# Kernel tuning notes

Hardware: AMD Instinct MI355X
Metric: run time of the kernel (lower is better)

## Reference

```python
import jax, jax.numpy as jnp
import numpy as np


def _lstm_layer(x, lengths, w_ih, w_hh, b):
    # x: [B, T, D], lengths: [B] int, w_ih/w_hh: [4H, D/H], b: [4H]
    B, T, D = x.shape
    H = w_hh.shape[1]
    # precompute input projection for all timesteps: [T, B, 4H]
    gx = (jnp.einsum('btd,gd->btg', x, w_ih) + b).transpose(1, 0, 2)
    tmask = (jnp.arange(T)[:, None] < lengths[None, :])[:, :, None]  # [T, B, 1]

    def step(carry, inp):
        c, h = carry
        g_x, m = inp
        gates = g_x + h @ w_hh.T  # [B, 4H]
        f, i, o, cg = jnp.split(gates, 4, axis=1)
        f = jax.nn.sigmoid(f)
        i = jax.nn.sigmoid(i)
        o = jax.nn.sigmoid(o)
        cg = jnp.tanh(cg)
        c_next = f * c + i * cg
        h_next = o * jnp.tanh(c_next)
        c_next = jnp.where(m, c_next, c)
        h_next = jnp.where(m, h_next, h)
        return (c_next, h_next), h_next

    c0 = jnp.zeros((B, H), dtype=x.dtype)
    h0 = jnp.zeros((B, H), dtype=x.dtype)
    (c_f, h_f), hs = jax.lax.scan(step, (c0, h0), (gx, tmask))
    return hs.transpose(1, 0, 2), (c_f, h_f)  # [B, T, H]


def reference(x, lengths, w_ih_0, w_hh_0, b_0, w_ih_1, w_hh_1, b_1):
    out0, (c0, h0) = _lstm_layer(x, lengths, w_ih_0, w_hh_0, b_0)
    out1, (c1, h1) = _lstm_layer(out0, lengths, w_ih_1, w_hh_1, b_1)
    c = jnp.stack([c0, c1], 0)  # [num_layers, B, H]
    h = jnp.stack([h0, h1], 0)
    return out1, (c, h)


def setup_inputs() -> dict:
    key = jax.random.key(0)
    ks = jax.random.split(key, 6)
    B, T, D, H = 32, 512, 1024, 1024
    s_in = 1.0 / np.sqrt(D)
    s_h = 1.0 / np.sqrt(H)
    return {
        'x': jax.random.normal(ks[0], (B, T, D), jnp.float32),
        'lengths': jax.random.randint(ks[1], (B,), 0, T).astype(jnp.int64),
        'w_ih_0': jax.random.normal(ks[2], (4 * H, D), jnp.float32) * s_in,
        'w_hh_0': jax.random.normal(ks[3], (4 * H, H), jnp.float32) * s_h,
        'b_0': jnp.zeros((4 * H,), jnp.float32),
        'w_ih_1': jax.random.normal(ks[4], (4 * H, H), jnp.float32) * s_h,
        'w_hh_1': jax.random.normal(ks[5], (4 * H, H), jnp.float32) * s_h,
        'b_1': jnp.zeros((4 * H,), jnp.float32),
    }
```

## Files before the change

### kernel.cpp

```cpp
#include <hip/hip_runtime.h>


#define BB 32
#define TT 512
#define HH 1024
#define NBLK 128

typedef float f32x4 __attribute__((ext_vector_type(4)));
typedef __bf16 bf16x8 __attribute__((ext_vector_type(8)));
typedef unsigned int u32x4 __attribute__((ext_vector_type(4)));

#define H0_OFF  0
#define H1_OFF  33554432
#define FL0_OFF 67108864
#define FL1_OFF (67108864 + 512)

#define LD16(d, a) asm volatile("global_load_dwordx4 %0, %1, off sc0 sc1" \
                                : "=v"(d) : "v"(a) : "memory")
#define ST16(a, v) asm volatile("global_store_dwordx4 %0, %1, off sc0 sc1" \
                                :: "v"(a), "v"(v) : "memory")

__device__ __forceinline__ float sigm(float x){ return 1.f/(1.f+__expf(-x)); }
__device__ __forceinline__ float tanh_s(float x){
  float a = fminf(fabsf(x), 20.f);
  float e = __expf(2.f*a);
  float r = (e-1.f)/(e+1.f);
  return x < 0.f ? -r : r;
}

__device__ __forceinline__ void waitflag(const int* fl, int lane, int need){
  const int* p = fl + 2*lane;
  for (;;){
    int a = __hip_atomic_load(p,   __ATOMIC_RELAXED, __HIP_MEMORY_SCOPE_AGENT);
    int b = __hip_atomic_load(p+1, __ATOMIC_RELAXED, __HIP_MEMORY_SCOPE_AGENT);
    if (!__any((a < need) | (b < need))) return;
    __builtin_amdgcn_s_sleep(1);
  }
}

__global__ __launch_bounds__(256, 1) void lstm2(
    const float* __restrict__ x, const int* __restrict__ l32,
    const float* __restrict__ wih0, const float* __restrict__ whh0, const float* __restrict__ b0,
    const float* __restrict__ wih1, const float* __restrict__ whh1, const float* __restrict__ b1,
    float* __restrict__ out, char* __restrict__ ws)
{
  extern __shared__ char smem[];
  float* redf = (float*)(smem + 131072);
  __bf16* hstage = (__bf16*)(smem + 149504);
  const int tid = threadIdx.x, bid = blockIdx.x;
  const int layer = bid >> 7, lb = bid & (NBLK-1), c0 = lb*8;
  const float* wih  = layer ? wih1 : wih0;
  const float* whh  = layer ? whh1 : whh0;
  const float* bias = layer ? b1 : b0;
  __bf16* h0b = (__bf16*)(ws + H0_OFF);
  __bf16* h1b = (__bf16*)(ws + H1_OFF);
  int* fl0 = (int*)(ws + FL0_OFF);
  int* fl1 = (int*)(ws + FL1_OFF);

  for (int idx = tid; idx < 32*1024; idx += 256){
    int m = idx >> 10, k = idx & (HH-1);
    int gr = (m >> 3)*HH + c0 + (m & 7);
    int off = m*2048 + ((k*2) ^ ((m & 15) << 4));
    *(__bf16*)(smem + off)         = (__bf16)wih[(size_t)gr*HH + k];
    *(__bf16*)(smem + 65536 + off) = (__bf16)whh[(size_t)gr*HH + k];
  }

  int odd = 0;
#pragma unroll
  for (int i = 1; i < 32; i += 2) odd |= l32[i];
  const int eb = tid >> 3, ec = tid & 7, cgl = c0 + ec;
  const int mylen = odd ? l32[eb] : l32[2*eb];
  float bias_r[4];
#pragma unroll
  for (int g = 0; g < 4; ++g) bias_r[g] = bias[g*HH + cgl];
  float c_st = 0.f, h_st = 0.f;

  const int lane = tid & 63, wid = tid >> 6;
  const int part = wid >> 1;
  const int kch  = wid & 1;
  const int col16 = lane & 15, kgrp = lane >> 4;
  const int axor = col16 << 4;
  const char* wbase = (const char*)smem + part*65536 + col16*2048 + kch*1024;
  float* wr = redf + wid*1152;
  const int kbase = kch*512 + kgrp*8;

  __syncthreads();

  for (int t = 0; t < TT; ++t){
    f32x4 acc00={0,0,0,0}, acc01={0,0,0,0}, acc10={0,0,0,0}, acc11={0,0,0,0};

    const __bf16* bsrc = nullptr;
    const float*  fsrc = nullptr;
    const int* fl = nullptr; int need = 0;
    if (layer == 0){
      if (part == 0) fsrc = x + (t << 10);
      else if (t > 0){ bsrc = h0b + ((size_t)(t-1) << 15); fl = fl0; need = t; }
    } else {
      if (part == 0){ bsrc = h0b + ((size_t)t << 15); fl = fl0; need = t+1; }
      else if (t > 0){ bsrc = h1b + ((size_t)(t-1) << 15); fl = fl1; need = t; }
    }
    if (fl) waitflag(fl, lane, need);

    if (bsrc){
      const char* pa = (const char*)(bsrc + col16*HH + kbase);
      const char* pb = (const char*)(bsrc + (16+col16)*HH + kbase);
      u32x4 ra[16], rb[16];
#pragma unroll
      for (int u = 0; u < 16; ++u){ LD16(ra[u], pa + u*64); LD16(rb[u], pb + u*64); }
      asm volatile("s_waitcnt vmcnt(0)" ::: "memory");
      __builtin_amdgcn_sched_barrier(0);
#pragma unroll
      for (int u = 0; u < 16; ++u){
        bf16x8 bv0 = __builtin_bit_cast(bf16x8, ra[u]);
        bf16x8 bv1 = __builtin_bit_cast(bf16x8, rb[u]);
        int ao = (u*64 + kgrp*16) ^ axor;
        bf16x8 a0 = *(const bf16x8*)(wbase + ao);
        bf16x8 a1 = *(const bf16x8*)(wbase + 32768 + ao);
        acc00 = __builtin_amdgcn_mfma_f32_16x16x32_bf16(a0, bv0, acc00, 0,0,0);
        acc01 = __builtin_amdgcn_mfma_f32_16x16x32_bf16(a0, bv1, acc01, 0,0,0);
        acc10 = __builtin_amdgcn_mfma_f32_16x16x32_bf16(a1, bv0, acc10, 0,0,0);
        acc11 = __builtin_amdgcn_mfma_f32_16x16x32_bf16(a1, bv1, acc11, 0,0,0);
      }
    } else if (fsrc){
      const float* p0 = fsrc + ((size_t)col16 << 19) + kbase;
      const float* p1 = fsrc + ((size_t)(16+col16) << 19) + kbase;
#pragma unroll 4
      for (int kb = 0; kb < 16; ++kb){
        float4 u0a = *(const float4*)(p0 + kb*32), u0b = *(const float4*)(p0 + kb*32 + 4);
        float4 u1a = *(const float4*)(p1 + kb*32), u1b = *(const float4*)(p1 + kb*32 + 4);
        bf16x8 bv0, bv1;
        bv0[0]=(__bf16)u0a.x; bv0[1]=(__bf16)u0a.y; bv0[2]=(__bf16)u0a.z; bv0[3]=(__bf16)u0a.w;
        bv0[4]=(__bf16)u0b.x; bv0[5]=(__bf16)u0b.y; bv0[6]=(__bf16)u0b.z; bv0[7]=(__bf16)u0b.w;
        bv1[0]=(__bf16)u1a.x; bv1[1]=(__bf16)u1a.y; bv1[2]=(__bf16)u1a.z; bv1[3]=(__bf16)u1a.w;
        bv1[4]=(__bf16)u1b.x; bv1[5]=(__bf16)u1b.y; bv1[6]=(__bf16)u1b.z; bv1[7]=(__bf16)u1b.w;
        int ao = (kb*64 + kgrp*16) ^ axor;
        bf16x8 a0 = *(const bf16x8*)(wbase + ao);
        bf16x8 a1 = *(const bf16x8*)(wbase + 32768 + ao);
        acc00 = __builtin_amdgcn_mfma_f32_16x16x32_bf16(a0, bv0, acc00, 0,0,0);
        acc01 = __builtin_amdgcn_mfma_f32_16x16x32_bf16(a0, bv1, acc01, 0,0,0);
        acc10 = __builtin_amdgcn_mfma_f32_16x16x32_bf16(a1, bv0, acc10, 0,0,0);
        acc11 = __builtin_amdgcn_mfma_f32_16x16x32_bf16(a1, bv1, acc11, 0,0,0);
      }
    }

    *(f32x4*)(wr + col16*36 + kgrp*4)           = acc00;
    *(f32x4*)(wr + (16+col16)*36 + kgrp*4)      = acc01;
    *(f32x4*)(wr + col16*36 + 16 + kgrp*4)      = acc10;
    *(f32x4*)(wr + (16+col16)*36 + 16 + kgrp*4) = acc11;
    __syncthreads();

    float vv[4];
#pragma unroll
    for (int g = 0; g < 4; ++g){
      int mi = eb*36 + g*8 + ec;
      vv[g] = redf[mi] + redf[1152+mi] + redf[2304+mi] + redf[3456+mi] + bias_r[g];
    }
    float fg = sigm(vv[0]), ig = sigm(vv[1]), og = sigm(vv[2]), gg = tanh_s(vv[3]);
    float cn = fg*c_st + ig*gg;
    float hn = og*tanh_s(cn);
    if (t < mylen){ c_st = cn; h_st = hn; }
    hstage[eb*8 + ec] = (__bf16)h_st;
    if (layer) out[((size_t)(eb*TT + t) << 10) + cgl] = h_st;
    __syncthreads();

    if (wid == 0){
      __bf16* hb = (layer ? h1b : h0b) + ((size_t)t << 15) + c0;
      if (lane < 32){
        u32x4 hv = *(const u32x4*)(hstage + lane*8);
        ST16(hb + (size_t)lane*HH, hv);
      }
      asm volatile("s_waitcnt vmcnt(0)" ::: "memory");
      if (lane == 0)
        __hip_atomic_store((layer ? fl1 : fl0) + lb, t+1,
                           __ATOMIC_RELAXED, __HIP_MEMORY_SCOPE_AGENT);
    }
  }

  const size_t OFFC = (size_t)BB*TT*HH;
  out[OFFC + (layer << 15) + (eb << 10) + cgl] = c_st;
  out[OFFC + ((2 + layer) << 15) + (eb << 10) + cgl] = h_st;
}

extern "C" void kernel_launch(void* const* d_in, const int* in_sizes, int n_in,
                              void* d_out, int out_size, void* d_ws, size_t ws_size,
                              hipStream_t stream) {
  const float* x    = (const float*)d_in[0];
  const int*   lens = (const int*)d_in[1];
  const float* wih0 = (const float*)d_in[2];
  const float* whh0 = (const float*)d_in[3];
  const float* b0   = (const float*)d_in[4];
  const float* wih1 = (const float*)d_in[5];
  const float* whh1 = (const float*)d_in[6];
  const float* b1   = (const float*)d_in[7];
  float* out = (float*)d_out;
  char* ws = (char*)d_ws;

  (void)hipMemsetAsync(ws + FL0_OFF, 0, 1024, stream);

  const int lds_bytes = 131072 + 4*1152*4 + 512;
  (void)hipFuncSetAttribute((const void*)lstm2,
                            hipFuncAttributeMaxDynamicSharedMemorySize, lds_bytes);
  lstm2<<<dim3(256), dim3(256), lds_bytes, stream>>>(
      x, lens, wih0, whh0, b0, wih1, whh1, b1, out, ws);
}
```

Before: 5.805 ms.

## Use per-timestep arrival counters, pre-converted bf16 input, and a ring buffer for layer-1 h

Replaces the per-block flag array, which every wave scanned across 128 entries, with one atomic counter per timestep. Each block increments the counter after publishing its slice of h, and waiters poll a single word until it reaches 128. A separate pre-pass converts x to bf16 in a [T,B,D] layout, so layer 0 reads x through the same bf16 MFMA path as h instead of doing strided fp32 loads and conversions inside the recurrent loop. Layer-1 hidden states go into a 4-slot ring with a padded row stride, and the data loads drop the sc0/sc1 coherence bits. That last change risks stale reads across caches, particularly for the reused ring slots.

```diff
diff --git a/kernel.cpp b/kernel.cpp
--- a/kernel.cpp
+++ b/kernel.cpp
@@ -5,18 +5,20 @@
 #define TT 512
 #define HH 1024
 #define NBLK 128
+#define TSTR 66048
 
 typedef float f32x4 __attribute__((ext_vector_type(4)));
 typedef __bf16 bf16x8 __attribute__((ext_vector_type(8)));
+typedef __bf16 bf16x4 __attribute__((ext_vector_type(4)));
 typedef unsigned int u32x4 __attribute__((ext_vector_type(4)));
 
-#define H0_OFF  0
-#define H1_OFF  33554432
-#define FL0_OFF 67108864
-#define FL1_OFF (67108864 + 512)
+#define H0_OFF   0
+#define H1R_OFF  33816576
+#define CNT_OFF  34080768
+#define XBF_OFF  34084864
 
-#define LD16(d, a) asm volatile("global_load_dwordx4 %0, %1, off sc0 sc1" \
-                                : "=v"(d) : "v"(a) : "memory")
+#define LDC16(d, a) asm volatile("global_load_dwordx4 %0, %1, off" \
+                                 : "=v"(d) : "v"(a) : "memory")
 #define ST16(a, v) asm volatile("global_store_dwordx4 %0, %1, off sc0 sc1" \
                                 :: "v"(a), "v"(v) : "memory")
 
@@ -27,19 +29,29 @@
   float r = (e-1.f)/(e+1.f);
   return x < 0.f ? -r : r;
 }
+__device__ __forceinline__ int ld_coh(const int* p){
+  int v;
+  asm volatile("global_load_dword %0, %1, off sc0 sc1\n\ts_waitcnt vmcnt(0)"
+               : "=v"(v) : "v"(p) : "memory");
+  return v;
+}
+__device__ __forceinline__ void poll128(const int* p){
+  while (ld_coh(p) < NBLK) __builtin_amdgcn_s_sleep(1);
+}
 
-__device__ __forceinline__ void waitflag(const int* fl, int lane, int need){
-  const int* p = fl + 2*lane;
-  for (;;){
-    int a = __hip_atomic_load(p,   __ATOMIC_RELAXED, __HIP_MEMORY_SCOPE_AGENT);
-    int b = __hip_atomic_load(p+1, __ATOMIC_RELAXED, __HIP_MEMORY_SCOPE_AGENT);
-    if (!__any((a < need) | (b < need))) return;
-    __builtin_amdgcn_s_sleep(1);
-  }
+__global__ __launch_bounds__(256) void xconv_kernel(const float* __restrict__ x,
+                                                    __bf16* __restrict__ xbf){
+  int i = blockIdx.x*256 + threadIdx.x;
+  int flat = i << 2;
+  int b = flat >> 19, t = (flat >> 10) & (TT-1), d = flat & (HH-1);
+  float4 v = *(const float4*)(x + flat);
+  bf16x4 o;
+  o[0]=(__bf16)v.x; o[1]=(__bf16)v.y; o[2]=(__bf16)v.z; o[3]=(__bf16)v.w;
+  *(bf16x4*)(xbf + ((t*BB + b) << 10) + d) = o;
 }
 
 __global__ __launch_bounds__(256, 1) void lstm2(
-    const float* __restrict__ x, const int* __restrict__ l32,
+    const int* __restrict__ l32,
     const float* __restrict__ wih0, const float* __restrict__ whh0, const float* __restrict__ b0,
     const float* __restrict__ wih1, const float* __restrict__ whh1, const float* __restrict__ b1,
     float* __restrict__ out, char* __restrict__ ws)
@@ -52,10 +64,11 @@
   const float* wih  = layer ? wih1 : wih0;
   const float* whh  = layer ? whh1 : whh0;
   const float* bias = layer ? b1 : b0;
-  __bf16* h0b = (__bf16*)(ws + H0_OFF);
-  __bf16* h1b = (__bf16*)(ws + H1_OFF);
-  int* fl0 = (int*)(ws + FL0_OFF);
-  int* fl1 = (int*)(ws + FL1_OFF);
+  char* h0 = ws + H0_OFF;
+  char* h1r = ws + H1R_OFF;
+  int* cnt0 = (int*)(ws + CNT_OFF);
+  int* cnt1 = cnt0 + 512;
+  const char* xb = ws + XBF_OFF;
 
   for (int idx = tid; idx < 32*1024; idx += 256){
     int m = idx >> 10, k = idx & (HH-1);
@@ -89,24 +102,23 @@
   for (int t = 0; t < TT; ++t){
     f32x4 acc00={0,0,0,0}, acc01={0,0,0,0}, acc10={0,0,0,0}, acc11={0,0,0,0};
 
-    const __bf16* bsrc = nullptr;
-    const float*  fsrc = nullptr;
-    const int* fl = nullptr; int need = 0;
+    const char* sb = nullptr;
+    const int* pollp = nullptr;
     if (layer == 0){
-      if (part == 0) fsrc = x + (t << 10);
-      else if (t > 0){ bsrc = h0b + ((size_t)(t-1) << 15); fl = fl0; need = t; }
+      if (part == 0) sb = xb + ((size_t)t << 16);
+      else if (t > 0){ sb = h0 + (size_t)(t-1)*TSTR; pollp = cnt0 + (t-1); }
     } else {
-      if (part == 0){ bsrc = h0b + ((size_t)t << 15); fl = fl0; need = t+1; }
-      else if (t > 0){ bsrc = h1b + ((size_t)(t-1) << 15); fl = fl1; need = t; }
+      if (part == 0){ sb = h0 + (size_t)t*TSTR; pollp = cnt0 + t; }
+      else if (t > 0){ sb = h1r + (size_t)((t-1)&3)*TSTR; pollp = cnt1 + (t-1); }
     }
-    if (fl) waitflag(fl, lane, need);
+    if (pollp) poll128(pollp);
 
-    if (bsrc){
-      const char* pa = (const char*)(bsrc + col16*HH + kbase);
-      const char* pb = (const char*)(bsrc + (16+col16)*HH + kbase);
+    if (sb){
+      const char* pa = sb + col16*2048 + kbase*2;
+      const char* pb = sb + (16+col16)*2048 + kbase*2;
       u32x4 ra[16], rb[16];
 #pragma unroll
-      for (int u = 0; u < 16; ++u){ LD16(ra[u], pa + u*64); LD16(rb[u], pb + u*64); }
+      for (int u = 0; u < 16; ++u){ LDC16(ra[u], pa + u*64); LDC16(rb[u], pb + u*64); }
       asm volatile("s_waitcnt vmcnt(0)" ::: "memory");
       __builtin_amdgcn_sched_barrier(0);
 #pragma unroll
@@ -114,26 +126,6 @@
         bf16x8 bv0 = __builtin_bit_cast(bf16x8, ra[u]);
         bf16x8 bv1 = __builtin_bit_cast(bf16x8, rb[u]);
         int ao = (u*64 + kgrp*16) ^ axor;
-        bf16x8 a0 = *(const bf16x8*)(wbase + ao);
-        bf16x8 a1 = *(const bf16x8*)(wbase + 32768 + ao);
-        acc00 = __builtin_amdgcn_mfma_f32_16x16x32_bf16(a0, bv0, acc00, 0,0,0);
-        acc01 = __builtin_amdgcn_mfma_f32_16x16x32_bf16(a0, bv1, acc01, 0,0,0);
-        acc10 = __builtin_amdgcn_mfma_f32_16x16x32_bf16(a1, bv0, acc10, 0,0,0);
-        acc11 = __builtin_amdgcn_mfma_f32_16x16x32_bf16(a1, bv1, acc11, 0,0,0);
-      }
-    } else if (fsrc){
-      const float* p0 = fsrc + ((size_t)col16 << 19) + kbase;
-      const float* p1 = fsrc + ((size_t)(16+col16) << 19) + kbase;
-#pragma unroll 4
-      for (int kb = 0; kb < 16; ++kb){
-        float4 u0a = *(const float4*)(p0 + kb*32), u0b = *(const float4*)(p0 + kb*32 + 4);
-        float4 u1a = *(const float4*)(p1 + kb*32), u1b = *(const float4*)(p1 + kb*32 + 4);
-        bf16x8 bv0, bv1;
-        bv0[0]=(__bf16)u0a.x; bv0[1]=(__bf16)u0a.y; bv0[2]=(__bf16)u0a.z; bv0[3]=(__bf16)u0a.w;
-        bv0[4]=(__bf16)u0b.x; bv0[5]=(__bf16)u0b.y; bv0[6]=(__bf16)u0b.z; bv0[7]=(__bf16)u0b.w;
-        bv1[0]=(__bf16)u1a.x; bv1[1]=(__bf16)u1a.y; bv1[2]=(__bf16)u1a.z; bv1[3]=(__bf16)u1a.w;
-        bv1[4]=(__bf16)u1b.x; bv1[5]=(__bf16)u1b.y; bv1[6]=(__bf16)u1b.z; bv1[7]=(__bf16)u1b.w;
-        int ao = (kb*64 + kgrp*16) ^ axor;
         bf16x8 a0 = *(const bf16x8*)(wbase + ao);
         bf16x8 a1 = *(const bf16x8*)(wbase + 32768 + ao);
         acc00 = __builtin_amdgcn_mfma_f32_16x16x32_bf16(a0, bv0, acc00, 0,0,0);
@@ -164,15 +156,15 @@
     __syncthreads();
 
     if (wid == 0){
-      __bf16* hb = (layer ? h1b : h0b) + ((size_t)t << 15) + c0;
+      char* hb = (layer ? (h1r + (size_t)(t&3)*TSTR) : (h0 + (size_t)t*TSTR)) + c0*2;
       if (lane < 32){
         u32x4 hv = *(const u32x4*)(hstage + lane*8);
-        ST16(hb + (size_t)lane*HH, hv);
+        ST16(hb + (size_t)lane*2048, hv);
       }
       asm volatile("s_waitcnt vmcnt(0)" ::: "memory");
       if (lane == 0)
-        __hip_atomic_store((layer ? fl1 : fl0) + lb, t+1,
-                           __ATOMIC_RELAXED, __HIP_MEMORY_SCOPE_AGENT);
+        __hip_atomic_fetch_add((layer ? cnt1 : cnt0) + t, 1,
+                               __ATOMIC_RELAXED, __HIP_MEMORY_SCOPE_AGENT);
     }
   }
 
@@ -195,11 +187,12 @@
   float* out = (float*)d_out;
   char* ws = (char*)d_ws;
 
-  (void)hipMemsetAsync(ws + FL0_OFF, 0, 1024, stream);
+  (void)hipMemsetAsync(ws + CNT_OFF, 0, 4096, stream);
+  xconv_kernel<<<dim3(16384), dim3(256), 0, stream>>>(x, (__bf16*)(ws + XBF_OFF));
 
   const int lds_bytes = 131072 + 4*1152*4 + 512;
   (void)hipFuncSetAttribute((const void*)lstm2,
                             hipFuncAttributeMaxDynamicSharedMemorySize, lds_bytes);
   lstm2<<<dim3(256), dim3(256), lds_bytes, stream>>>(
-      x, lens, wih0, whh0, b0, wih1, whh1, b1, out, ws);
+      lens, wih0, whh0, b0, wih1, whh1, b1, out, ws);
 }
```

Result: faster. 5.084 ms (-12.4%).

## Hold LSTM weights in registers and store hidden state in per-block contiguous slices

Applied to the files above, without the earlier changes.

Each wave now keeps its bf16 weight fragments resident in VGPRs instead of reading them from swizzled LDS every timestep, so the step loop no longer issues LDS weight loads. The inter-block hidden-state buffer is re-laid out so each block's 32x8 output is a contiguous 512-byte chunk. That makes the publish store coalesced and lets consumers read 16-byte pieces that map directly onto MFMA B operands. Hidden-state loads drop the sc0/sc1 cache bits and are consumed in four staged vmcnt waits, so MFMAs overlap the remaining loads; the output store also moves after the flag publish. The trade is heavy VGPR pressure and reliance on never-reused addresses staying coherent without the cache bits.

```diff
diff --git a/kernel.cpp b/kernel.cpp
--- a/kernel.cpp
+++ b/kernel.cpp
@@ -5,20 +5,23 @@
 #define TT 512
 #define HH 1024
 #define NBLK 128
+#define SLICE 65536
 
 typedef float f32x4 __attribute__((ext_vector_type(4)));
 typedef __bf16 bf16x8 __attribute__((ext_vector_type(8)));
 typedef unsigned int u32x4 __attribute__((ext_vector_type(4)));
-
-#define H0_OFF  0
-#define H1_OFF  33554432
-#define FL0_OFF 67108864
-#define FL1_OFF (67108864 + 512)
-
-#define LD16(d, a) asm volatile("global_load_dwordx4 %0, %1, off sc0 sc1" \
-                                : "=v"(d) : "v"(a) : "memory")
+typedef int i32x2 __attribute__((ext_vector_type(2)));
+
+#define H0_OFF 0
+#define H1_OFF ((size_t)TT * SLICE)
+#define FL_OFF ((size_t)2 * TT * SLICE)
+
+#define LDC16(d, a) asm volatile("global_load_dwordx4 %0, %1, off" \
+                                 : "=v"(d) : "v"(a) : "memory")
 #define ST16(a, v) asm volatile("global_store_dwordx4 %0, %1, off sc0 sc1" \
                                 :: "v"(a), "v"(v) : "memory")
+#define WAITV(N) asm volatile("s_waitcnt vmcnt(" #N ")" ::: "memory"); \
+                 __builtin_amdgcn_sched_barrier(0)
 
 __device__ __forceinline__ float sigm(float x){ return 1.f/(1.f+__expf(-x)); }
 __device__ __forceinline__ float tanh_s(float x){
@@ -27,15 +30,21 @@
   float r = (e-1.f)/(e+1.f);
   return x < 0.f ? -r : r;
 }
-
-__device__ __forceinline__ void waitflag(const int* fl, int lane, int need){
+__device__ __forceinline__ void pollge(const int* fl, int lane, int need){
   const int* p = fl + 2*lane;
   for (;;){
-    int a = __hip_atomic_load(p,   __ATOMIC_RELAXED, __HIP_MEMORY_SCOPE_AGENT);
-    int b = __hip_atomic_load(p+1, __ATOMIC_RELAXED, __HIP_MEMORY_SCOPE_AGENT);
-    if (!__any((a < need) | (b < need))) return;
+    i32x2 v;
+    asm volatile("global_load_dwordx2 %0, %1, off sc0 sc1\n\ts_waitcnt vmcnt(0)"
+                 : "=v"(v) : "v"(p) : "memory");
+    if (!__any((v[0] < need) | (v[1] < need))) return;
     __builtin_amdgcn_s_sleep(1);
   }
+}
+__device__ __forceinline__ bf16x8 cvt8(float4 a, float4 b){
+  bf16x8 r;
+  r[0]=(__bf16)a.x; r[1]=(__bf16)a.y; r[2]=(__bf16)a.z; r[3]=(__bf16)a.w;
+  r[4]=(__bf16)b.x; r[5]=(__bf16)b.y; r[6]=(__bf16)b.z; r[7]=(__bf16)b.w;
+  return r;
 }
 
 __global__ __launch_bounds__(256, 1) void lstm2(
@@ -44,26 +53,15 @@
     const float* __restrict__ wih1, const float* __restrict__ whh1, const float* __restrict__ b1,
     float* __restrict__ out, char* __restrict__ ws)
 {
-  extern __shared__ char smem[];
-  float* redf = (float*)(smem + 131072);
-  __bf16* hstage = (__bf16*)(smem + 149504);
+  __shared__ float redf[4*1152];
+  __shared__ __bf16 hstage[BB*8];
   const int tid = threadIdx.x, bid = blockIdx.x;
   const int layer = bid >> 7, lb = bid & (NBLK-1), c0 = lb*8;
-  const float* wih  = layer ? wih1 : wih0;
-  const float* whh  = layer ? whh1 : whh0;
   const float* bias = layer ? b1 : b0;
-  __bf16* h0b = (__bf16*)(ws + H0_OFF);
-  __bf16* h1b = (__bf16*)(ws + H1_OFF);
-  int* fl0 = (int*)(ws + FL0_OFF);
-  int* fl1 = (int*)(ws + FL1_OFF);
-
-  for (int idx = tid; idx < 32*1024; idx += 256){
-    int m = idx >> 10, k = idx & (HH-1);
-    int gr = (m >> 3)*HH + c0 + (m & 7);
-    int off = m*2048 + ((k*2) ^ ((m & 15) << 4));
-    *(__bf16*)(smem + off)         = (__bf16)wih[(size_t)gr*HH + k];
-    *(__bf16*)(smem + 65536 + off) = (__bf16)whh[(size_t)gr*HH + k];
-  }
+  char* h0 = ws + H0_OFF;
+  char* h1 = ws + H1_OFF;
+  int* fl0 = (int*)(ws + FL_OFF);
+  int* fl1 = fl0 + NBLK;
 
   int odd = 0;
 #pragma unroll
@@ -79,67 +77,65 @@
   const int part = wid >> 1;
   const int kch  = wid & 1;
   const int col16 = lane & 15, kgrp = lane >> 4;
-  const int axor = col16 << 4;
-  const char* wbase = (const char*)smem + part*65536 + col16*2048 + kch*1024;
   float* wr = redf + wid*1152;
   const int kbase = kch*512 + kgrp*8;
 
-  __syncthreads();
+  const float* wsel = part ? (layer ? whh1 : whh0) : (layer ? wih1 : wih0);
+  const int m0 = col16, m1 = 16 + col16;
+  const float* ws0 = wsel + (size_t)((m0>>3)*HH + c0 + (m0&7))*HH + kbase;
+  const float* ws1 = wsel + (size_t)((m1>>3)*HH + c0 + (m1&7))*HH + kbase;
+  bf16x8 wa[16], wb[16];
+#pragma unroll
+  for (int u = 0; u < 16; ++u){
+    wa[u] = cvt8(*(const float4*)(ws0 + u*32), *(const float4*)(ws0 + u*32 + 4));
+    wb[u] = cvt8(*(const float4*)(ws1 + u*32), *(const float4*)(ws1 + u*32 + 4));
+  }
 
   for (int t = 0; t < TT; ++t){
     f32x4 acc00={0,0,0,0}, acc01={0,0,0,0}, acc10={0,0,0,0}, acc11={0,0,0,0};
 
-    const __bf16* bsrc = nullptr;
-    const float*  fsrc = nullptr;
+    const char* sb = nullptr;
+    const float* fsrc = nullptr;
     const int* fl = nullptr; int need = 0;
     if (layer == 0){
       if (part == 0) fsrc = x + (t << 10);
-      else if (t > 0){ bsrc = h0b + ((size_t)(t-1) << 15); fl = fl0; need = t; }
+      else if (t > 0){ sb = h0 + (size_t)(t-1)*SLICE; fl = fl0; need = t; }
     } else {
-      if (part == 0){ bsrc = h0b + ((size_t)t << 15); fl = fl0; need = t+1; }
-      else if (t > 0){ bsrc = h1b + ((size_t)(t-1) << 15); fl = fl1; need = t; }
-    }
-    if (fl) waitflag(fl, lane, need);
-
-    if (bsrc){
-      const char* pa = (const char*)(bsrc + col16*HH + kbase);
-      const char* pb = (const char*)(bsrc + (16+col16)*HH + kbase);
+      if (part == 0){ sb = h0 + (size_t)t*SLICE; fl = fl0; need = t+1; }
+      else if (t > 0){ sb = h1 + (size_t)(t-1)*SLICE; fl = fl1; need = t; }
+    }
+    if (fl) pollge(fl, lane, need);
+
+    if (sb){
+      const char* bbase = sb + (size_t)(kch*64 + kgrp)*512 + col16*16;
       u32x4 ra[16], rb[16];
 #pragma unroll
-      for (int u = 0; u < 16; ++u){ LD16(ra[u], pa + u*64); LD16(rb[u], pb + u*64); }
-      asm volatile("s_waitcnt vmcnt(0)" ::: "memory");
-      __builtin_amdgcn_sched_barrier(0);
-#pragma unroll
       for (int u = 0; u < 16; ++u){
-        bf16x8 bv0 = __builtin_bit_cast(bf16x8, ra[u]);
-        bf16x8 bv1 = __builtin_bit_cast(bf16x8, rb[u]);
-        int ao = (u*64 + kgrp*16) ^ axor;
-        bf16x8 a0 = *(const bf16x8*)(wbase + ao);
-        bf16x8 a1 = *(const bf16x8*)(wbase + 32768 + ao);
-        acc00 = __builtin_amdgcn_mfma_f32_16x16x32_bf16(a0, bv0, acc00, 0,0,0);
-        acc01 = __builtin_amdgcn_mfma_f32_16x16x32_bf16(a0, bv1, acc01, 0,0,0);
-        acc10 = __builtin_amdgcn_mfma_f32_16x16x32_bf16(a1, bv0, acc10, 0,0,0);
-        acc11 = __builtin_amdgcn_mfma_f32_16x16x32_bf16(a1, bv1, acc11, 0,0,0);
-      }
+        LDC16(ra[u], bbase + u*2048);
+        LDC16(rb[u], bbase + u*2048 + 256);
+      }
+#define MMQ(u) { bf16x8 bv0 = __builtin_bit_cast(bf16x8, ra[u]); \
+                 bf16x8 bv1 = __builtin_bit_cast(bf16x8, rb[u]); \
+  acc00 = __builtin_amdgcn_mfma_f32_16x16x32_bf16(wa[u], bv0, acc00, 0,0,0); \
+  acc01 = __builtin_amdgcn_mfma_f32_16x16x32_bf16(wa[u], bv1, acc01, 0,0,0); \
+  acc10 = __builtin_amdgcn_mfma_f32_16x16x32_bf16(wb[u], bv0, acc10, 0,0,0); \
+  acc11 = __builtin_amdgcn_mfma_f32_16x16x32_bf16(wb[u], bv1, acc11, 0,0,0); }
+      WAITV(24); MMQ(0);  MMQ(1);  MMQ(2);  MMQ(3);
+      WAITV(16); MMQ(4);  MMQ(5);  MMQ(6);  MMQ(7);
+      WAITV(8);  MMQ(8);  MMQ(9);  MMQ(10); MMQ(11);
+      WAITV(0);  MMQ(12); MMQ(13); MMQ(14); MMQ(15);
+#undef MMQ
     } else if (fsrc){
       const float* p0 = fsrc + ((size_t)col16 << 19) + kbase;
       const float* p1 = fsrc + ((size_t)(16+col16) << 19) + kbase;
 #pragma unroll 4
-      for (int kb = 0; kb < 16; ++kb){
-        float4 u0a = *(const float4*)(p0 + kb*32), u0b = *(const float4*)(p0 + kb*32 + 4);
-        float4 u1a = *(const float4*)(p1 + kb*32), u1b = *(const float4*)(p1 + kb*32 + 4);
-        bf16x8 bv0, bv1;
-        bv0[0]=(__bf16)u0a.x; bv0[1]=(__bf16)u0a.y; bv0[2]=(__bf16)u0a.z; bv0[3]=(__bf16)u0a.w;
-        bv0[4]=(__bf16)u0b.x; bv0[5]=(__bf16)u0b.y; bv0[6]=(__bf16)u0b.z; bv0[7]=(__bf16)u0b.w;
-        bv1[0]=(__bf16)u1a.x; bv1[1]=(__bf16)u1a.y; bv1[2]=(__bf16)u1a.z; bv1[3]=(__bf16)u1a.w;
-        bv1[4]=(__bf16)u1b.x; bv1[5]=(__bf16)u1b.y; bv1[6]=(__bf16)u1b.z; bv1[7]=(__bf16)u1b.w;
-        int ao = (kb*64 + kgrp*16) ^ axor;
-        bf16x8 a0 = *(const bf16x8*)(wbase + ao);
-        bf16x8 a1 = *(const bf16x8*)(wbase + 32768 + ao);
-        acc00 = __builtin_amdgcn_mfma_f32_16x16x32_bf16(a0, bv0, acc00, 0,0,0);
-        acc01 = __builtin_amdgcn_mfma_f32_16x16x32_bf16(a0, bv1, acc01, 0,0,0);
-        acc10 = __builtin_amdgcn_mfma_f32_16x16x32_bf16(a1, bv0, acc10, 0,0,0);
-        acc11 = __builtin_amdgcn_mfma_f32_16x16x32_bf16(a1, bv1, acc11, 0,0,0);
+      for (int u = 0; u < 16; ++u){
+        bf16x8 bv0 = cvt8(*(const float4*)(p0 + u*32), *(const float4*)(p0 + u*32 + 4));
+        bf16x8 bv1 = cvt8(*(const float4*)(p1 + u*32), *(const float4*)(p1 + u*32 + 4));
+        acc00 = __builtin_amdgcn_mfma_f32_16x16x32_bf16(wa[u], bv0, acc00, 0,0,0);
+        acc01 = __builtin_amdgcn_mfma_f32_16x16x32_bf16(wa[u], bv1, acc01, 0,0,0);
+        acc10 = __builtin_amdgcn_mfma_f32_16x16x32_bf16(wb[u], bv0, acc10, 0,0,0);
+        acc11 = __builtin_amdgcn_mfma_f32_16x16x32_bf16(wb[u], bv1, acc11, 0,0,0);
       }
     }
 
@@ -159,21 +155,24 @@
     float cn = fg*c_st + ig*gg;
     float hn = og*tanh_s(cn);
     if (t < mylen){ c_st = cn; h_st = hn; }
-    hstage[eb*8 + ec] = (__bf16)h_st;
-    if (layer) out[((size_t)(eb*TT + t) << 10) + cgl] = h_st;
+    hstage[tid] = (__bf16)h_st;
     __syncthreads();
 
     if (wid == 0){
-      __bf16* hb = (layer ? h1b : h0b) + ((size_t)t << 15) + c0;
+      char* hb = (layer ? h1 : h0) + (size_t)t*SLICE + lb*512;
       if (lane < 32){
         u32x4 hv = *(const u32x4*)(hstage + lane*8);
-        ST16(hb + (size_t)lane*HH, hv);
+        ST16(hb + lane*16, hv);
       }
       asm volatile("s_waitcnt vmcnt(0)" ::: "memory");
-      if (lane == 0)
-        __hip_atomic_store((layer ? fl1 : fl0) + lb, t+1,
-                           __ATOMIC_RELAXED, __HIP_MEMORY_SCOPE_AGENT);
-    }
+      if (lane == 0){
+        int* fp = (layer ? fl1 : fl0) + lb;
+        int val = t + 1;
+        asm volatile("global_store_dword %0, %1, off sc0 sc1"
+                     :: "v"(fp), "v"(val) : "memory");
+      }
+    }
+    if (layer) out[((size_t)(eb*TT + t) << 10) + cgl] = h_st;
   }
 
   const size_t OFFC = (size_t)BB*TT*HH;
@@ -195,11 +194,8 @@
   float* out = (float*)d_out;
   char* ws = (char*)d_ws;
 
-  (void)hipMemsetAsync(ws + FL0_OFF, 0, 1024, stream);
-
-  const int lds_bytes = 131072 + 4*1152*4 + 512;
-  (void)hipFuncSetAttribute((const void*)lstm2,
-                            hipFuncAttributeMaxDynamicSharedMemorySize, lds_bytes);
-  lstm2<<<dim3(256), dim3(256), lds_bytes, stream>>>(
+  (void)hipMemsetAsync(ws + FL_OFF, 0, 1024, stream);
+
+  lstm2<<<dim3(256), dim3(256), 0, stream>>>(
       x, lens, wih0, whh0, b0, wih1, whh1, b1, out, ws);
 }
```

Result: slower. 12.84 ms (+121.2%).
